# Kernel tuning notes

Hardware: AMD Instinct MI355X
Metric: run time of the kernel (lower is better)

The kernel has to match this reference:

```python
import jax, jax.numpy as jnp
import numpy as np
import math

B, S, HID = 2, 1024, 2048
N_HEAD, N_KV = 16, 4
HEAD = HID // N_HEAD          # 128
N_REP = N_HEAD // N_KV        # 4


def setup_inputs() -> dict:
    key = jax.random.key(0)
    ks = jax.random.split(key, 5)
    x = jax.random.normal(ks[0], (B, S, HID), dtype=jnp.float32)
    # realistic RoPE tables: freqs over half dim, duplicated (rotate_half convention)
    inv_freq = 1.0 / (10000.0 ** (np.arange(0, HEAD, 2, dtype=np.float32) / HEAD))
    t = np.arange(S, dtype=np.float32)
    freqs = np.outer(t, inv_freq)                    # [S, HEAD/2]
    emb = np.concatenate([freqs, freqs], axis=-1)    # [S, HEAD]
    cos = jnp.asarray(np.cos(emb), dtype=jnp.float32)
    sin = jnp.asarray(np.sin(emb), dtype=jnp.float32)
    sc = 0.02
    wq = jax.random.normal(ks[1], (HID, HID), dtype=jnp.float32) * sc
    wk = jax.random.normal(ks[2], (HID, N_KV * HEAD), dtype=jnp.float32) * sc
    wv = jax.random.normal(ks[3], (HID, N_KV * HEAD), dtype=jnp.float32) * sc
    wo = jax.random.normal(ks[4], (HID, HID), dtype=jnp.float32) * sc
    return {"x": x, "cos": cos, "sin": sin, "wq": wq, "wk": wk, "wv": wv, "wo": wo}


def _rotate_half(t):
    h = t.shape[-1] // 2
    return jnp.concatenate([-t[..., h:], t[..., :h]], axis=-1)


def reference(x, cos, sin, wq, wk, wv, wo):
    b, s, _ = x.shape
    q = (x @ wq).reshape(b, s, N_HEAD, HEAD)   # [B,S,H,D]
    k = (x @ wk).reshape(b, s, N_KV, HEAD)     # [B,S,Kv,D]
    v = (x @ wv).reshape(b, s, N_KV, HEAD)
    # RoPE: cos/sin [S,D] -> [S,1,D], broadcasts over batch and heads
    c = cos[:s, None, :]
    sn = sin[:s, None, :]
    q = q * c + _rotate_half(q) * sn
    k = k * c + _rotate_half(k) * sn
    # GQA: repeat kv heads to match query heads
    k = jnp.repeat(k, N_REP, axis=2)           # [B,S,H,D]
    v = jnp.repeat(v, N_REP, axis=2)
    q = q.transpose(0, 2, 1, 3)                # [B,H,S,D]
    k = k.transpose(0, 2, 1, 3)
    v = v.transpose(0, 2, 1, 3)
    scores = jnp.einsum("bhqd,bhkd->bhqk", q, k) / math.sqrt(HEAD)
    causal = jnp.triu(jnp.full((s, s), -jnp.inf, dtype=scores.dtype), k=1)
    scores = scores + causal[None, None, :, :]
    probs = jax.nn.softmax(scores.astype(jnp.float32), axis=-1).astype(q.dtype)
    out = jnp.einsum("bhqk,bhkd->bhqd", probs, v)   # [B,H,S,D]
    out = out.transpose(0, 2, 1, 3).reshape(b, s, N_HEAD * HEAD)
    return out @ wo
```

## Files before the change

kernel.cpp:

```cpp
#include <hip/hip_runtime.h>
#include <hip/hip_bf16.h>
#include <math.h>
#include <stdint.h>

#define BATCH 2
#define SEQ   1024
#define HID   2048
#define NH    16
#define NKV   4
#define HEAD  128
#define MROWS (BATCH*SEQ)
#define QSC   0.08838834764831845f

typedef _Float16 f16;
typedef _Float16 f16x8 __attribute__((ext_vector_type(8)));
typedef __fp16   h16x2 __attribute__((ext_vector_type(2)));
typedef float    f32x4 __attribute__((ext_vector_type(4)));

__device__ __forceinline__ void glds16(const void* g, void* l) {
    __builtin_amdgcn_global_load_lds(
        (const __attribute__((address_space(1))) void*)g,
        (__attribute__((address_space(3))) void*)l, 16, 0, 0);
}

__device__ __forceinline__ f32x4 mfma16(f16x8 a, f16x8 b, f32x4 c) {
    return __builtin_amdgcn_mfma_f32_16x16x32_f16(a, b, c, 0, 0, 0);
}

__global__ __launch_bounds__(256)
void cvt_f32_f16(const float* __restrict__ in, f16* __restrict__ out) {
    int i = blockIdx.x * 256 + threadIdx.x;
    float4 v = ((const float4*)in)[i];
    union { ushort4 u; f16 h[4]; } o;
    o.h[0] = (f16)v.x; o.h[1] = (f16)v.y; o.h[2] = (f16)v.z; o.h[3] = (f16)v.w;
    ((ushort4*)out)[i] = o.u;
}

__global__ __launch_bounds__(256)
void transW(const float* __restrict__ w0, const float* __restrict__ w1,
            const float* __restrict__ w2, f16* __restrict__ out,
            int c1, int c2, int ld0, int ld1, int ld2) {
    __shared__ float t[64][65];
    const int n0 = blockIdx.x * 64, k0 = blockIdx.y * 64;
    const float* W; int ld, cb;
    if (n0 < c1)      { W = w0; ld = ld0; cb = 0;  }
    else if (n0 < c2) { W = w1; ld = ld1; cb = c1; }
    else              { W = w2; ld = ld2; cb = c2; }
    const int tr = threadIdx.x >> 4, tc = threadIdx.x & 15;
    #pragma unroll
    for (int i = 0; i < 4; ++i) {
        int row = tr * 4 + i;
        float4 v = *(const float4*)&W[(size_t)(k0 + row) * ld + (n0 - cb) + tc * 4];
        t[row][tc*4+0] = v.x; t[row][tc*4+1] = v.y;
        t[row][tc*4+2] = v.z; t[row][tc*4+3] = v.w;
    }
    __syncthreads();
    #pragma unroll
    for (int i = 0; i < 4; ++i) {
        int nrow = tr * 4 + i;
        union { ushort4 u; f16 h[4]; } o;
        o.h[0] = (f16)t[tc*4+0][nrow]; o.h[1] = (f16)t[tc*4+1][nrow];
        o.h[2] = (f16)t[tc*4+2][nrow]; o.h[3] = (f16)t[tc*4+3][nrow];
        *(ushort4*)&out[(size_t)(n0 + nrow) * 2048 + k0 + tc * 4] = o.u;
    }
}

template<int MODE>
__global__ __launch_bounds__(256, 2)
void gemm16(const f16* __restrict__ A, const f16* __restrict__ Bt,
            const float* __restrict__ cosp, const float* __restrict__ sinp,
            f16* __restrict__ Oq, f16* __restrict__ Ok, f16* __restrict__ Ov,
            float* __restrict__ Of)
{
    __shared__ f16 As[128 * 64];
    __shared__ f16 Bs[128 * 64];
    const int tid   = threadIdx.x;
    const int lane  = tid & 63;
    const int wid   = tid >> 6;
    const int col_l = lane & 15;
    const int hi    = lane >> 4;
    const int m0 = blockIdx.y * 128;
    const int n0 = blockIdx.x * 128;

    f32x4 acc[2][8];
    #pragma unroll
    for (int mt = 0; mt < 2; ++mt)
        #pragma unroll
        for (int nt = 0; nt < 8; ++nt)
            acc[mt][nt] = (f32x4){0.f, 0.f, 0.f, 0.f};

    for (int kt = 0; kt < 32; ++kt) {
        __syncthreads();
        #pragma unroll
        for (int j = 0; j < 4; ++j) {
            int gidx = j * 256 + tid;
            int r = gidx >> 3, g = gidx & 7;
            int gs = (g ^ (r & 7)) << 3;
            glds16(A  + (size_t)(m0 + r) * 2048 + kt * 64 + gs,
                   (char*)As + (size_t)(j * 256 + (wid << 6)) * 16);
            glds16(Bt + (size_t)(n0 + r) * 2048 + kt * 64 + gs,
                   (char*)Bs + (size_t)(j * 256 + (wid << 6)) * 16);
        }
        asm volatile("s_waitcnt vmcnt(0)" ::: "memory");
        __syncthreads();

        #pragma unroll
        for (int ks = 0; ks < 2; ++ks) {
            int gr = (ks << 2) | hi;
            int ar0 = wid * 32 + col_l;
            int ar1 = ar0 + 16;
            f16x8 a0 = *(const f16x8*)&As[ar0 * 64 + ((gr ^ (ar0 & 7)) << 3)];
            f16x8 a1 = *(const f16x8*)&As[ar1 * 64 + ((gr ^ (ar1 & 7)) << 3)];
            #pragma unroll
            for (int nt = 0; nt < 8; ++nt) {
                int br = nt * 16 + col_l;
                f16x8 b = *(const f16x8*)&Bs[br * 64 + ((gr ^ (br & 7)) << 3)];
                acc[0][nt] = mfma16(a0, b, acc[0][nt]);
                acc[1][nt] = mfma16(a1, b, acc[1][nt]);
            }
        }
    }

    if (MODE == 0) {
        #pragma unroll
        for (int mt = 0; mt < 2; ++mt)
            #pragma unroll
            for (int r = 0; r < 4; ++r) {
                int grow = m0 + wid * 32 + mt * 16 + hi * 4 + r;
                #pragma unroll
                for (int nt = 0; nt < 8; ++nt)
                    Of[(size_t)grow * 2048 + n0 + nt * 16 + col_l] = acc[mt][nt][r];
            }
    } else if (n0 < 2048) {
        #pragma unroll
        for (int mt = 0; mt < 2; ++mt)
            #pragma unroll
            for (int r = 0; r < 4; ++r) {
                int grow = m0 + wid * 32 + mt * 16 + hi * 4 + r;
                int srow = grow & (SEQ - 1);
                #pragma unroll
                for (int nt = 0; nt < 4; ++nt) {
                    int d = nt * 16 + col_l;
                    float lo = acc[mt][nt][r], hv = acc[mt][nt + 4][r];
                    float cl = cosp[srow * HEAD + d],      sl = sinp[srow * HEAD + d];
                    float ch = cosp[srow * HEAD + d + 64], sh = sinp[srow * HEAD + d + 64];
                    Oq[(size_t)grow * 2048 + n0 + d]      = (f16)((lo * cl - hv * sl) * QSC);
                    Oq[(size_t)grow * 2048 + n0 + d + 64] = (f16)((hv * ch + lo * sh) * QSC);
                }
            }
    } else if (n0 < 2560) {
        #pragma unroll
        for (int mt = 0; mt < 2; ++mt)
            #pragma unroll
            for (int r = 0; r < 4; ++r) {
                int grow = m0 + wid * 32 + mt * 16 + hi * 4 + r;
                int srow = grow & (SEQ - 1);
                #pragma unroll
                for (int nt = 0; nt < 4; ++nt) {
                    int kc = (n0 - 2048) + nt * 16 + col_l;
                    int d  = kc & 127;
                    float lo = acc[mt][nt][r], hv = acc[mt][nt + 4][r];
                    float cl = cosp[srow * HEAD + d],      sl = sinp[srow * HEAD + d];
                    float ch = cosp[srow * HEAD + d + 64], sh = sinp[srow * HEAD + d + 64];
                    Ok[(size_t)grow * 512 + kc]      = (f16)(lo * cl - hv * sl);
                    Ok[(size_t)grow * 512 + kc + 64] = (f16)(hv * ch + lo * sh);
                }
            }
    } else {
        #pragma unroll
        for (int mt = 0; mt < 2; ++mt) {
            int grow0 = m0 + wid * 32 + mt * 16 + hi * 4;
            int bb = grow0 >> 10, s0 = grow0 & (SEQ - 1);
            #pragma unroll
            for (int nt = 0; nt < 8; ++nt) {
                int vcol = (n0 - 2560) + nt * 16 + col_l;
                int kvh = vcol >> 7, d = vcol & 127;
                union { ushort4 u; f16 h[4]; } pv;
                #pragma unroll
                for (int r = 0; r < 4; ++r) pv.h[r] = (f16)acc[mt][nt][r];
                *(ushort4*)&Ov[(size_t)((bb * 4 + kvh) * 128 + d) * 1024 + s0] = pv.u;
            }
        }
    }
}

__global__ __launch_bounds__(256, 2)
void attn16(const f16* __restrict__ q16, const f16* __restrict__ k16,
            const f16* __restrict__ vT, f16* __restrict__ attnb)
{
    __shared__ f16 Ks[32 * 128];
    __shared__ f16 Vs[128 * 32];

    const int tid   = threadIdx.x;
    const int lane  = tid & 63;
    const int wid   = tid >> 6;
    const int col_l = lane & 15;
    const int hi    = lane >> 4;

    const int bx = blockIdx.x;
    const int qt = 15 - (bx >> 5);
    const int bh = bx & 31;
    const int b  = bh >> 4;
    const int h  = bh & 15;
    const int kv = h >> 2;
    const int qrow = qt * 64 + wid * 16 + col_l;

    f16x8 qf[4];
    {
        const f16* qp = q16 + (size_t)(b * SEQ + qrow) * 2048 + h * 128 + hi * 8;
        #pragma unroll
        for (int ks = 0; ks < 4; ++ks) qf[ks] = *(const f16x8*)&qp[ks * 32];
    }
    const f16* vTg = vT + (size_t)(b * 4 + kv) * 128 * 1024;

    f32x4 O[8];
    #pragma unroll
    for (int dt = 0; dt < 8; ++dt) O[dt] = (f32x4){0.f, 0.f, 0.f, 0.f};
    float mrun = -INFINITY, lrun = 0.f;

    const int ntiles = 2 * (qt + 1);
    for (int kt = 0; kt < ntiles; ++kt) {
        __syncthreads();
        #pragma unroll
        for (int j = 0; j < 2; ++j) {
            int gidx = j * 256 + tid;
            int r = gidx >> 4, g = gidx & 15;
            glds16(k16 + (size_t)(b * SEQ + kt * 32 + r) * 512 + kv * 128 + ((g ^ (r & 7)) << 3),
                   (char*)Ks + (size_t)(j * 256 + (wid << 6)) * 16);
            int d = gidx >> 2, g2 = gidx & 3;
            glds16(vTg + (size_t)d * 1024 + kt * 32 + ((g2 ^ (d & 3)) << 3),
                   (char*)Vs + (size_t)(j * 256 + (wid << 6)) * 16);
        }
        asm volatile("s_waitcnt vmcnt(0)" ::: "memory");
        __syncthreads();

        f32x4 S0 = (f32x4){0.f,0.f,0.f,0.f}, S1 = (f32x4){0.f,0.f,0.f,0.f};
        #pragma unroll
        for (int ks = 0; ks < 4; ++ks) {
            int gr = (ks << 2) | hi;
            int r0 = col_l, r1 = col_l + 16;
            f16x8 kf0 = *(const f16x8*)&Ks[r0 * 128 + ((gr ^ (r0 & 7)) << 3)];
            f16x8 kf1 = *(const f16x8*)&Ks[r1 * 128 + ((gr ^ (r1 & 7)) << 3)];
            S0 = mfma16(kf0, qf[ks], S0);
            S1 = mfma16(kf1, qf[ks], S1);
        }
        float p[8];
        p[0]=S0[0]; p[1]=S0[1]; p[2]=S0[2]; p[3]=S0[3];
        p[4]=S1[0]; p[5]=S1[1]; p[6]=S1[2]; p[7]=S1[3];

        #pragma unroll
        for (int sl = 0; sl < 8; ++sl) {
            int kk = kt * 32 + (sl >> 2) * 16 + hi * 4 + (sl & 3);
            if (kk > qrow) p[sl] = -INFINITY;
        }

        float mt = p[0];
        #pragma unroll
        for (int sl = 1; sl < 8; ++sl) mt = fmaxf(mt, p[sl]);
        mt = fmaxf(mt, __shfl_xor(mt, 16));
        mt = fmaxf(mt, __shfl_xor(mt, 32));
        float mnew = fmaxf(mrun, mt);
        float corr = __expf(mrun - mnew);
        mrun = mnew;
        float ps = 0.f;
        #pragma unroll
        for (int sl = 0; sl < 8; ++sl) { p[sl] = __expf(p[sl] - mnew); ps += p[sl]; }
        ps += __shfl_xor(ps, 16);
        ps += __shfl_xor(ps, 32);
        lrun = lrun * corr + ps;

        union U2 { h16x2 h; int i; };
        int pk[4];
        { U2 u; u.h = __builtin_amdgcn_cvt_pkrtz(p[0], p[1]); pk[0] = u.i; }
        { U2 u; u.h = __builtin_amdgcn_cvt_pkrtz(p[2], p[3]); pk[1] = u.i; }
        { U2 u; u.h = __builtin_amdgcn_cvt_pkrtz(p[4], p[5]); pk[2] = u.i; }
        { U2 u; u.h = __builtin_amdgcn_cvt_pkrtz(p[6], p[7]); pk[3] = u.i; }
        union UA { f16x8 v; int i[4]; } ua;
        #pragma unroll
        for (int j = 0; j < 4; ++j) {
            int srcl = col_l + 16 * ((2 * hi + (j >> 1)) & 3);
            int v0 = __builtin_amdgcn_ds_bpermute(srcl << 2, pk[j & 1]);
            int v1 = __builtin_amdgcn_ds_bpermute(srcl << 2, pk[(j & 1) + 2]);
            ua.i[j] = (hi >= 2) ? v1 : v0;
        }

        float cb[4];
        #pragma unroll
        for (int r = 0; r < 4; ++r)
            cb[r] = __int_as_float(__builtin_amdgcn_ds_bpermute((hi * 4 + r) << 2,
                                                                __float_as_int(corr)));
        #pragma unroll
        for (int dt = 0; dt < 8; ++dt) {
            O[dt][0] *= cb[0]; O[dt][1] *= cb[1];
            O[dt][2] *= cb[2]; O[dt][3] *= cb[3];
        }

        #pragma unroll
        for (int dt = 0; dt < 8; ++dt) {
            int vr = dt * 16 + col_l;
            f16x8 vf = *(const f16x8*)&Vs[vr * 32 + (((hi) ^ (vr & 3)) << 3)];
            O[dt] = mfma16(ua.v, vf, O[dt]);
        }
    }

    float linv = 1.f / lrun;
    float lb[4];
    #pragma unroll
    for (int r = 0; r < 4; ++r)
        lb[r] = __int_as_float(__builtin_amdgcn_ds_bpermute((hi * 4 + r) << 2,
                                                            __float_as_int(linv)));
    #pragma unroll
    for (int dt = 0; dt < 8; ++dt)
        #pragma unroll
        for (int r = 0; r < 4; ++r) {
            int row = b * SEQ + qt * 64 + wid * 16 + hi * 4 + r;
            attnb[(size_t)row * 2048 + h * 128 + dt * 16 + col_l] = (f16)(O[dt][r] * lb[r]);
        }
}

extern "C" void kernel_launch(void* const* d_in, const int* in_sizes, int n_in,
                              void* d_out, int out_size, void* d_ws, size_t ws_size,
                              hipStream_t stream)
{
    const float* x    = (const float*)d_in[0];
    const float* cosp = (const float*)d_in[1];
    const float* sinp = (const float*)d_in[2];
    const float* wq   = (const float*)d_in[3];
    const float* wk   = (const float*)d_in[4];
    const float* wv   = (const float*)d_in[5];
    const float* wo   = (const float*)d_in[6];
    float* out = (float*)d_out;

    char* ws = (char*)d_ws;
    f16* x16    = (f16*)(ws);
    f16* attn16v= (f16*)(ws);
    f16* Wqkvt  = (f16*)(ws + 8388608);
    f16* Wot    = (f16*)(ws + 8388608);
    f16* q16    = (f16*)(ws + 20971520);
    f16* k16    = (f16*)(ws + 29360128);
    f16* vT     = (f16*)(ws + 31457280);

    cvt_f32_f16<<<4096, 256, 0, stream>>>(x, x16);

    transW<<<dim3(48, 32), 256, 0, stream>>>(wq, wk, wv, Wqkvt, 2048, 2560, 2048, 512, 512);

    gemm16<1><<<dim3(24, 16), 256, 0, stream>>>(x16, Wqkvt, cosp, sinp,
                                                q16, k16, vT, nullptr);

    transW<<<dim3(32, 32), 256, 0, stream>>>(wo, wo, wo, Wot, 2048, 2048, 2048, 2048, 2048);

    attn16<<<dim3(512), 256, 0, stream>>>(q16, k16, vT, attn16v);

    gemm16<0><<<dim3(16, 16), 256, 0, stream>>>(attn16v, Wot, nullptr, nullptr,
                                                nullptr, nullptr, nullptr, out);
}
```

Baseline: 224.8 us.

## Double-buffer LDS tiles in GEMM and attention kernels to overlap loads with MFMA

```diff
diff --git a/kernel.cpp b/kernel.cpp
--- a/kernel.cpp
+++ b/kernel.cpp
@@ -72,8 +72,8 @@
             f16* __restrict__ Oq, f16* __restrict__ Ok, f16* __restrict__ Ov,
             float* __restrict__ Of)
 {
-    __shared__ f16 As[128 * 64];
-    __shared__ f16 Bs[128 * 64];
+    __shared__ f16 As[2][128 * 64];
+    __shared__ f16 Bs[2][128 * 64];
     const int tid   = threadIdx.x;
     const int lane  = tid & 63;
     const int wid   = tid >> 6;
@@ -89,35 +89,48 @@
         for (int nt = 0; nt < 8; ++nt)
             acc[mt][nt] = (f32x4){0.f, 0.f, 0.f, 0.f};
 
-    for (int kt = 0; kt < 32; ++kt) {
-        __syncthreads();
+    auto stage = [&](int buf, int kt) {
         #pragma unroll
         for (int j = 0; j < 4; ++j) {
             int gidx = j * 256 + tid;
             int r = gidx >> 3, g = gidx & 7;
             int gs = (g ^ (r & 7)) << 3;
             glds16(A  + (size_t)(m0 + r) * 2048 + kt * 64 + gs,
-                   (char*)As + (size_t)(j * 256 + (wid << 6)) * 16);
+                   (char*)&As[buf][0] + (size_t)(j * 256 + (wid << 6)) * 16);
             glds16(Bt + (size_t)(n0 + r) * 2048 + kt * 64 + gs,
-                   (char*)Bs + (size_t)(j * 256 + (wid << 6)) * 16);
-        }
-        asm volatile("s_waitcnt vmcnt(0)" ::: "memory");
-        __syncthreads();
+                   (char*)&Bs[buf][0] + (size_t)(j * 256 + (wid << 6)) * 16);
+        }
+    };
+
+    stage(0, 0);
+    asm volatile("s_waitcnt vmcnt(0)" ::: "memory");
+    __syncthreads();
+
+    int cur = 0;
+    #pragma unroll 1
+    for (int kt = 0; kt < 32; ++kt) {
+        if (kt < 31) stage(cur ^ 1, kt + 1);
 
         #pragma unroll
         for (int ks = 0; ks < 2; ++ks) {
             int gr = (ks << 2) | hi;
             int ar0 = wid * 32 + col_l;
             int ar1 = ar0 + 16;
-            f16x8 a0 = *(const f16x8*)&As[ar0 * 64 + ((gr ^ (ar0 & 7)) << 3)];
-            f16x8 a1 = *(const f16x8*)&As[ar1 * 64 + ((gr ^ (ar1 & 7)) << 3)];
+            f16x8 a0 = *(const f16x8*)&As[cur][ar0 * 64 + ((gr ^ (ar0 & 7)) << 3)];
+            f16x8 a1 = *(const f16x8*)&As[cur][ar1 * 64 + ((gr ^ (ar1 & 7)) << 3)];
             #pragma unroll
             for (int nt = 0; nt < 8; ++nt) {
                 int br = nt * 16 + col_l;
-                f16x8 b = *(const f16x8*)&Bs[br * 64 + ((gr ^ (br & 7)) << 3)];
+                f16x8 b = *(const f16x8*)&Bs[cur][br * 64 + ((gr ^ (br & 7)) << 3)];
                 acc[0][nt] = mfma16(a0, b, acc[0][nt]);
                 acc[1][nt] = mfma16(a1, b, acc[1][nt]);
             }
+        }
+
+        if (kt < 31) {
+            asm volatile("s_waitcnt vmcnt(0)" ::: "memory");
+            __syncthreads();
+            cur ^= 1;
         }
     }
 
@@ -188,8 +201,8 @@
 void attn16(const f16* __restrict__ q16, const f16* __restrict__ k16,
             const f16* __restrict__ vT, f16* __restrict__ attnb)
 {
-    __shared__ f16 Ks[32 * 128];
-    __shared__ f16 Vs[128 * 32];
+    __shared__ f16 Ks[2][32 * 128];
+    __shared__ f16 Vs[2][128 * 32];
 
     const int tid   = threadIdx.x;
     const int lane  = tid & 63;
@@ -198,7 +211,7 @@
     const int hi    = lane >> 4;
 
     const int bx = blockIdx.x;
-    const int qt = 15 - (bx >> 5);
+    const int qt = (bx < 256) ? (15 - (bx >> 5)) : ((bx - 256) >> 5);
     const int bh = bx & 31;
     const int b  = bh >> 4;
     const int h  = bh & 15;
@@ -213,34 +226,41 @@
     }
     const f16* vTg = vT + (size_t)(b * 4 + kv) * 128 * 1024;
 
-    f32x4 O[8];
-    #pragma unroll
-    for (int dt = 0; dt < 8; ++dt) O[dt] = (f32x4){0.f, 0.f, 0.f, 0.f};
-    float mrun = -INFINITY, lrun = 0.f;
-
-    const int ntiles = 2 * (qt + 1);
-    for (int kt = 0; kt < ntiles; ++kt) {
-        __syncthreads();
+    auto stage = [&](int buf, int kt) {
         #pragma unroll
         for (int j = 0; j < 2; ++j) {
             int gidx = j * 256 + tid;
             int r = gidx >> 4, g = gidx & 15;
             glds16(k16 + (size_t)(b * SEQ + kt * 32 + r) * 512 + kv * 128 + ((g ^ (r & 7)) << 3),
-                   (char*)Ks + (size_t)(j * 256 + (wid << 6)) * 16);
+                   (char*)&Ks[buf][0] + (size_t)(j * 256 + (wid << 6)) * 16);
             int d = gidx >> 2, g2 = gidx & 3;
             glds16(vTg + (size_t)d * 1024 + kt * 32 + ((g2 ^ (d & 3)) << 3),
-                   (char*)Vs + (size_t)(j * 256 + (wid << 6)) * 16);
-        }
-        asm volatile("s_waitcnt vmcnt(0)" ::: "memory");
-        __syncthreads();
+                   (char*)&Vs[buf][0] + (size_t)(j * 256 + (wid << 6)) * 16);
+        }
+    };
+
+    f32x4 O[8];
+    #pragma unroll
+    for (int dt = 0; dt < 8; ++dt) O[dt] = (f32x4){0.f, 0.f, 0.f, 0.f};
+    float mrun = -INFINITY, lrun = 0.f;
+
+    const int ntiles = 2 * (qt + 1);
+    stage(0, 0);
+    asm volatile("s_waitcnt vmcnt(0)" ::: "memory");
+    __syncthreads();
+
+    int cur = 0;
+    #pragma unroll 1
+    for (int kt = 0; kt < ntiles; ++kt) {
+        if (kt + 1 < ntiles) stage(cur ^ 1, kt + 1);
 
         f32x4 S0 = (f32x4){0.f,0.f,0.f,0.f}, S1 = (f32x4){0.f,0.f,0.f,0.f};
         #pragma unroll
         for (int ks = 0; ks < 4; ++ks) {
             int gr = (ks << 2) | hi;
             int r0 = col_l, r1 = col_l + 16;
-            f16x8 kf0 = *(const f16x8*)&Ks[r0 * 128 + ((gr ^ (r0 & 7)) << 3)];
-            f16x8 kf1 = *(const f16x8*)&Ks[r1 * 128 + ((gr ^ (r1 & 7)) << 3)];
+            f16x8 kf0 = *(const f16x8*)&Ks[cur][r0 * 128 + ((gr ^ (r0 & 7)) << 3)];
+            f16x8 kf1 = *(const f16x8*)&Ks[cur][r1 * 128 + ((gr ^ (r1 & 7)) << 3)];
             S0 = mfma16(kf0, qf[ks], S0);
             S1 = mfma16(kf1, qf[ks], S1);
         }
@@ -298,8 +318,14 @@
         #pragma unroll
         for (int dt = 0; dt < 8; ++dt) {
             int vr = dt * 16 + col_l;
-            f16x8 vf = *(const f16x8*)&Vs[vr * 32 + (((hi) ^ (vr & 3)) << 3)];
+            f16x8 vf = *(const f16x8*)&Vs[cur][vr * 32 + (((hi) ^ (vr & 3)) << 3)];
             O[dt] = mfma16(ua.v, vf, O[dt]);
+        }
+
+        if (kt + 1 < ntiles) {
+            asm volatile("s_waitcnt vmcnt(0)" ::: "memory");
+            __syncthreads();
+            cur ^= 1;
         }
     }
 
```

Result: no change. 227.5 us (+1.2%).
